# Performance work log

Hardware: AMD Instinct MI355X
Metric: run time of the kernel (lower is better)

Reference implementation:

```python
import jax, jax.numpy as jnp
import numpy as np

B, N, NPOINT, NSAMPLE = 8, 8192, 2048, 32
RADIUS = 0.4
C_IN = 64
MLP = [64, 64, 128]
EPS = 1e-5
BIG = 1e10


def setup_inputs() -> dict:
    key = jax.random.key(0)
    ks = jax.random.split(key, 2 + 4 * len(MLP))
    inp = {
        'xyz': jax.random.normal(ks[0], (B, N, 3), jnp.float32),
        'features': jax.random.normal(ks[1], (B, C_IN, N), jnp.float32),
    }
    last_c = C_IN + 3
    j = 2
    for i, out_c in enumerate(MLP):
        inp[f'w{i}'] = jax.random.normal(ks[j], (out_c, last_c), jnp.float32) * (1.0 / np.sqrt(last_c)); j += 1
        inp[f'b{i}'] = jax.random.normal(ks[j], (out_c,), jnp.float32) * 0.01; j += 1
        inp[f'g{i}'] = 1.0 + 0.01 * jax.random.normal(ks[j], (out_c,), jnp.float32); j += 1
        inp[f'bt{i}'] = 0.01 * jax.random.normal(ks[j], (out_c,), jnp.float32); j += 1
        last_c = out_c
    return inp


def fps(xyz, m):
    # Farthest point sampling; deterministic start at index 0 (torch uses randint).
    b, n, _ = xyz.shape

    def step(carry, _):
        dist, far = carry
        centroid = jnp.take_along_axis(xyz, far[:, None, None], axis=1)  # [B,1,3]
        d = jnp.sum((xyz - centroid) ** 2, axis=-1)                      # [B,N]
        dist = jnp.minimum(dist, d)
        new_far = jnp.argmax(dist, axis=1)
        return (dist, new_far), far

    init = (jnp.full((b, n), BIG, xyz.dtype), jnp.zeros((b,), jnp.int32))
    _, idxs = jax.lax.scan(step, init, None, length=m)
    return jnp.transpose(idxs)  # [B,m]


def ball_query(xyz, centroids, radius, k):
    # Euclidean cdist via the (a-b)^2 = a^2 + b^2 - 2ab expansion.
    x2 = jnp.sum(xyz * xyz, axis=-1)            # [B,N]
    c2 = jnp.sum(centroids * centroids, axis=-1)  # [B,M]
    d2 = c2[:, :, None] + x2[:, None, :] - 2.0 * jnp.einsum('bmd,bnd->bmn', centroids, xyz)
    d = jnp.sqrt(jnp.maximum(d2, 0.0))           # [B,M,N]
    dm = jnp.where(d <= radius, d, BIG)
    _, idx = jax.lax.top_k(-dm, k)               # k smallest distances
    return idx                                   # [B,M,K]


def gather_points(x, idx):
    # x: [B,N,C], idx: [B,M,K] -> [B,M,K,C]
    b = x.shape[0]
    return x[jnp.arange(b)[:, None, None], idx]


def reference(xyz, features, w0, b0, g0, bt0, w1, b1, g1, bt1, w2, b2, g2, bt2):
    idx = fps(xyz, NPOINT)                                   # [B,M]
    new_xyz = jnp.take_along_axis(xyz, idx[:, :, None], axis=1)  # [B,M,3]
    knn_idx = ball_query(xyz, new_xyz, RADIUS, NSAMPLE)      # [B,M,K]
    grouped_xyz = gather_points(xyz, knn_idx)                # [B,M,K,3]
    grouped_xyz_norm = grouped_xyz - new_xyz[:, :, None, :]
    grouped_feat = gather_points(jnp.transpose(features, (0, 2, 1)), knn_idx)  # [B,M,K,C]
    feat = jnp.concatenate([grouped_xyz_norm, grouped_feat], axis=-1)          # [B,M,K,C+3]

    for w, b, g, bt in ((w0, b0, g0, bt0), (w1, b1, g1, bt1), (w2, b2, g2, bt2)):
        feat = jnp.einsum('bmkc,oc->bmko', feat, w) + b      # 1x1 conv
        mu = jnp.mean(feat, axis=(0, 1, 2))                  # BN, training-mode batch stats
        var = jnp.mean((feat - mu) ** 2, axis=(0, 1, 2))
        feat = (feat - mu) * jax.lax.rsqrt(var + EPS) * g + bt
        feat = jax.nn.relu(feat)

    new_feat = jnp.max(feat, axis=2)                         # max over neighbors -> [B,M,C_out]
    return new_xyz, jnp.transpose(new_feat, (0, 2, 1))       # [B,M,3], [B,C_out,M]
```

## Files before the change

kernel.cpp:

```cpp
#include <hip/hip_runtime.h>
#include <hip/hip_bf16.h>
#include <stdint.h>

typedef unsigned short u16;
typedef unsigned int   u32;
typedef unsigned long long u64;
typedef float v2f __attribute__((ext_vector_type(2)));
typedef __attribute__((ext_vector_type(8))) short bf16x8;
typedef __attribute__((ext_vector_type(4))) float f32x4;

#define B_    8
#define N_    8192
#define M_    2048
#define NS_   32
#define CIN_  64
#define ROWS_ (B_*M_*NS_)
#define BIGF  1e10f
#define EPSF  1e-5f
#define INV_ROWS (1.0f/524288.0f)

__device__ __forceinline__ u16 f2bf(float f){
  u32 x=__float_as_uint(f);
  return (u16)((x + 0x7FFFu + ((x>>16)&1u))>>16);
}
__device__ __forceinline__ float bf2f(u16 u){ return __uint_as_float(((u32)u)<<16); }

__device__ __forceinline__ u64 wave_max_key(u64 k){
#define DPP_LVL(CTRL) { \
    u32 lo_=(u32)__builtin_amdgcn_update_dpp(0,(int)(u32)k,(CTRL),0xF,0xF,true); \
    u32 hi_=(u32)__builtin_amdgcn_update_dpp(0,(int)(u32)(k>>32),(CTRL),0xF,0xF,true); \
    u64 o_=((u64)hi_<<32)|(u64)lo_; \
    k=(o_>k)?o_:k; }
  DPP_LVL(0x111)
  DPP_LVL(0x112)
  DPP_LVL(0x114)
  DPP_LVL(0x118)
  DPP_LVL(0x142)
  DPP_LVL(0x143)
#undef DPP_LVL
  return k;
}

__global__ __launch_bounds__(256) void k_prep(
    const float* w0,const float* b0,const float* g0,const float* bt0,
    const float* w1,const float* b1,const float* g1,const float* bt1,
    const float* w2,const float* b2,const float* g2,const float* bt2,
    float* Wt0,float* Wt1,float* Wt2,
    float* biasf,float* gf,float* btf,float* stats,
    u16* Wb1h, u16* Wb1l)
{
  int tid=threadIdx.x;
  for (int i=tid;i<768;i+=256) stats[i]=0.f;
  for (int i=tid;i<67*64;i+=256){ int c=i>>6,o=i&63;  Wt0[c*64+o]=w0[o*67+c]; }
  for (int i=tid;i<64*64;i+=256){ int c=i>>6,o=i&63;  Wt1[c*64+o]=w1[o*64+c]; }
  for (int i=tid;i<64*128;i+=256){int c=i>>7,o=i&127; Wt2[c*128+o]=w2[o*64+c]; }
  for (int i=tid;i<4096;i+=256){
    int e=i&7, lane=(i>>3)&63, k0=(i>>9)&1, tn=i>>10;
    int col = tn*16 + (lane&15);
    int k   = k0*32 + ((lane>>4)&3)*8 + e;
    float v = w1[col*64 + k];
    u16 hib = f2bf(v);
    float lo = v - bf2f(hib);
    Wb1h[i] = hib;
    Wb1l[i] = f2bf(lo);
  }
  if (tid<64){
    biasf[0*128+tid]=b0[tid]; gf[0*128+tid]=g0[tid]; btf[0*128+tid]=bt0[tid];
    biasf[1*128+tid]=b1[tid]; gf[1*128+tid]=g1[tid]; btf[1*128+tid]=bt1[tid];
  }
  if (tid<128){
    biasf[2*128+tid]=b2[tid]; gf[2*128+tid]=g2[tid]; btf[2*128+tid]=bt2[tid];
  }
}

__global__ __launch_bounds__(256) void k_tr(const float* __restrict__ feats, u16* __restrict__ featT)
{
  __shared__ float t[64][65];
  int bb=blockIdx.y, n0=blockIdx.x*64, tid=threadIdx.x;
  int a=tid&63, q=tid>>6;
  const float* fp = feats + (size_t)bb*CIN_*N_;
  #pragma unroll
  for (int s=0;s<16;s++){ int c=q*16+s; t[c][a]=fp[(size_t)c*N_ + n0 + a]; }
  __syncthreads();
  u16* op = featT + (size_t)bb*N_*CIN_;
  #pragma unroll
  for (int s=0;s<16;s++){ int n=q*16+s; op[(size_t)(n0+n)*CIN_ + a] = f2bf(t[a][n]); }
}

__global__ __launch_bounds__(512) void k_fps(const float* __restrict__ xyz,
                                             float* __restrict__ nxyz, float* __restrict__ out0)
{
#pragma clang fp contract(off)
  __shared__ float sx[N_], sy[N_], sz[N_];
  __shared__ int sidx[M_];
  __shared__ u64 skey[2][8];
  int b=blockIdx.x, tid=threadIdx.x;
  const float* xp = xyz + (size_t)b*N_*3;
  for (int i=tid;i<N_;i+=512){ sx[i]=xp[i*3]; sy[i]=xp[i*3+1]; sz[i]=xp[i*3+2]; }
  __syncthreads();
  v2f px[8],py[8],pz[8],md[8];
  int base = tid*16;
  #pragma unroll
  for (int p=0;p<8;p++){
    px[p]=*(const v2f*)&sx[base+2*p];
    py[p]=*(const v2f*)&sy[base+2*p];
    pz[p]=*(const v2f*)&sz[base+2*p];
    v2f m0; m0[0]=BIGF; m0[1]=BIGF; md[p]=m0;
  }
  u32 invb = 0xFFFFFFFFu - (u32)base;
  int far=0;
  int lane=tid&63, wv=tid>>6;
  for (int step=0; step<M_; step++){
    if (tid==0) sidx[step]=far;
    float cxs=sx[far], cys=sy[far], czs=sz[far];
    v2f cx; cx[0]=cxs; cx[1]=cxs;
    v2f cy; cy[0]=cys; cy[1]=cys;
    v2f cz; cz[0]=czs; cz[1]=czs;
    u64 kb=0;
    #pragma unroll
    for (int p=0;p<8;p++){
      v2f dx=px[p]-cx, dy=py[p]-cy, dz=pz[p]-cz;
      v2f d=(dx*dx+dy*dy)+dz*dz;
      v2f m=__builtin_elementwise_min(md[p],d);
      md[p]=m;
      u64 k0=((u64)__float_as_uint(m[0])<<32)|(u64)(invb-(u32)(2*p));
      u64 k1=((u64)__float_as_uint(m[1])<<32)|(u64)(invb-(u32)(2*p+1));
      u64 kp=(k1>k0)?k1:k0;
      kb=(kp>kb)?kp:kb;
    }
    kb = wave_max_key(kb);
    int par = step & 1;
    if (lane==63) skey[par][wv]=kb;
    __syncthreads();
    u64 a0=skey[par][0],a1=skey[par][1],a2=skey[par][2],a3=skey[par][3];
    u64 a4=skey[par][4],a5=skey[par][5],a6=skey[par][6],a7=skey[par][7];
    a0=(a1>a0)?a1:a0; a2=(a3>a2)?a3:a2; a4=(a5>a4)?a5:a4; a6=(a7>a6)?a7:a6;
    a0=(a2>a0)?a2:a0; a4=(a6>a4)?a6:a4;
    a0=(a4>a0)?a4:a0;
    far = (int)(0xFFFFFFFFu - (u32)(a0 & 0xFFFFFFFFull));
  }
  for (int i=tid;i<M_;i+=512){
    int id = sidx[i];
    float x=sx[id], y=sy[id], z=sz[id];
    size_t o=(size_t)(b*M_+i)*3;
    nxyz[o]=x; nxyz[o+1]=y; nxyz[o+2]=z;
    out0[o]=x; out0[o+1]=y; out0[o+2]=z;
  }
}

#define BQCAP 512
__global__ __launch_bounds__(512) void k_bq(const float* __restrict__ xyz, const float* __restrict__ nxyz,
                                            int* __restrict__ knn)
{
  __shared__ float4 sP[N_];
  __shared__ float candd[8][BQCAP];
  __shared__ u16  candi[8][BQCAP];
  int tid=threadIdx.x;
  int cid0 = blockIdx.x*8;
  int b = cid0 >> 11;
  const float* xp = xyz + (size_t)b*N_*3;
  for (int i=tid;i<N_;i+=512){
    float x=xp[i*3], y=xp[i*3+1], z=xp[i*3+2];
    float x2 = __fmul_rn(x,x);
    x2 = __fadd_rn(x2, __fmul_rn(y,y));
    x2 = __fadd_rn(x2, __fmul_rn(z,z));
    sP[i]=make_float4(x,y,z,x2);
  }
  __syncthreads();
  int w=tid>>6, lane=tid&63;
  int cid = cid0 + w;
  float cx=nxyz[(size_t)cid*3], cy=nxyz[(size_t)cid*3+1], cz=nxyz[(size_t)cid*3+2];
  float c2 = __fmul_rn(cx,cx);
  c2 = __fadd_rn(c2, __fmul_rn(cy,cy));
  c2 = __fadd_rn(c2, __fmul_rn(cz,cz));
  int cnt=0;
  for (int i0=0;i0<N_;i0+=64){
    int i=i0+lane;
    float4 p=sP[i];
    float dot = __fmul_rn(cx,p.x);
    dot = __fadd_rn(dot, __fmul_rn(cy,p.y));
    dot = __fadd_rn(dot, __fmul_rn(cz,p.z));
    float d2 = __fsub_rn(__fadd_rn(c2,p.w), __fmul_rn(2.0f,dot));
    float d = sqrtf(fmaxf(d2,0.f));
    bool in = (d <= 0.4f);
    u64 msk = __ballot(in);
    int pos = cnt + __popcll(msk & ((1ull<<lane)-1ull));
    if (in && pos<BQCAP){ candd[w][pos]=d; candi[w][pos]=(u16)i; }
    cnt += __popcll(msk);
  }
  int R = cnt<BQCAP ? cnt : BQCAP;
  int* kout = knn + (size_t)cid*NS_;
  if (R >= NS_){
    for (int s=0;s<NS_;s++){
      u64 kb = ~0ull;
      for (int j=lane;j<R;j+=64){
        float v=candd[w][j];
        u64 k = ((u64)__float_as_uint(v)<<32) | (u64)(u32)j;
        kb = (k<kb)?k:kb;
      }
      u64 inv = wave_max_key(~kb);
      if (lane==63){
        u64 kw = ~inv;
        int bpp = (int)(u32)(kw & 0xFFFFFFFFull);
        kout[s]=candi[w][bpp];
        candd[w][bpp]=3e38f;
      }
    }
  } else {
    if (lane<R) kout[lane]=candi[w][lane];
    int need = NS_-R, slot = R;
    for (int i0=0; i0<N_ && need>0; i0+=64){
      int i=i0+lane;
      float4 p=sP[i];
      float dot = __fmul_rn(cx,p.x);
      dot = __fadd_rn(dot, __fmul_rn(cy,p.y));
      dot = __fadd_rn(dot, __fmul_rn(cz,p.z));
      float d2 = __fsub_rn(__fadd_rn(c2,p.w), __fmul_rn(2.0f,dot));
      float d = sqrtf(fmaxf(d2,0.f));
      bool in = (d <= 0.4f);
      u64 mm = __ballot(!in);
      while (mm && need>0){
        int bpos = __ffsll((long long)mm)-1;
        if (lane==0) kout[slot] = i0+bpos;
        slot++; need--;
        mm &= mm-1;
      }
    }
  }
}

__global__ __launch_bounds__(256) void k_mm0(const float* __restrict__ xyz, const u16* __restrict__ featT,
                                             const int* __restrict__ knn, const float* __restrict__ nxyz,
                                             const float* __restrict__ Wt0, const float* __restrict__ biasf,
                                             u16* __restrict__ Y0)
{
  __shared__ u16 Xs[256*70];
  __shared__ float Wl[67*64];
  int tid=threadIdx.x;
  for (int i=tid;i<67*64;i+=256) Wl[i]=Wt0[i];
  int base = blockIdx.x*256;
  {
    int row = base + tid;
    int bm  = row >> 5;
    int b   = row >> 16;
    int n   = knn[row];
    const float* cp = nxyz + (size_t)bm*3;
    const float* xp = xyz + ((size_t)b*N_ + n)*3;
    u16* xr = &Xs[tid*70];
    xr[0]=f2bf(xp[0]-cp[0]);
    xr[1]=f2bf(xp[1]-cp[1]);
    xr[2]=f2bf(xp[2]-cp[2]);
    const uint4* fp = (const uint4*)(featT + ((size_t)b*N_ + n)*CIN_);
    #pragma unroll
    for (int i=0;i<8;i++){
      uint4 v=fp[i];
      u16* d = xr + 3 + i*8;
      d[0]=(u16)(v.x&0xFFFFu); d[1]=(u16)(v.x>>16);
      d[2]=(u16)(v.y&0xFFFFu); d[3]=(u16)(v.y>>16);
      d[4]=(u16)(v.z&0xFFFFu); d[5]=(u16)(v.z>>16);
      d[6]=(u16)(v.w&0xFFFFu); d[7]=(u16)(v.w>>16);
    }
  }
  __syncthreads();
  int g=tid>>7, rt=tid&127;
  float acc0[32], acc1[32];
  #pragma unroll
  for (int j=0;j<32;j++){ acc0[j]=0.f; acc1[j]=0.f; }
  const u16* xa=&Xs[rt*70];
  const u16* xb=&Xs[(rt+128)*70];
  for (int c=0;c<67;c++){
    float a=bf2f(xa[c]);
    float bx=bf2f(xb[c]);
    const float4* wr=(const float4*)&Wl[c*64 + g*32];
    #pragma unroll
    for (int o=0;o<8;o++){
      float4 wv=wr[o];
      acc0[o*4+0]+=a*wv.x;  acc0[o*4+1]+=a*wv.y;  acc0[o*4+2]+=a*wv.z;  acc0[o*4+3]+=a*wv.w;
      acc1[o*4+0]+=bx*wv.x; acc1[o*4+1]+=bx*wv.y; acc1[o*4+2]+=bx*wv.z; acc1[o*4+3]+=bx*wv.w;
    }
  }
  float bb[32];
  #pragma unroll
  for (int j=0;j<32;j++) bb[j]=biasf[g*32+j];
  u16* y0p = Y0 + ((size_t)(base+rt))*64 + g*32;
  u16* y1p = Y0 + ((size_t)(base+rt+128))*64 + g*32;
  #pragma unroll
  for (int j=0;j<32;j++){
    y0p[j]=f2bf(acc0[j]+bb[j]);
    y1p[j]=f2bf(acc1[j]+bb[j]);
  }
}

template<int C>
__global__ __launch_bounds__(256) void k_stats(const u16* __restrict__ Y, float* __restrict__ statsOut)
{
  __shared__ float sred[4][128];
  int tid=threadIdx.x;
  int c0=(tid&7)*8;
  int rg=tid>>3;
  float s[8], ss[8];
  #pragma unroll
  for (int k=0;k<8;k++){ s[k]=0.f; ss[k]=0.f; }
  for (size_t r=(size_t)blockIdx.x*32+rg; r<ROWS_; r+=(size_t)gridDim.x*32){
    uint4 v=*(const uint4*)&Y[r*64+c0];
    u32 a[4]={v.x,v.y,v.z,v.w};
    #pragma unroll
    for (int q=0;q<4;q++){
      float lo=bf2f((u16)(a[q]&0xFFFFu));
      float hi=bf2f((u16)(a[q]>>16));
      s[q*2]+=lo;   ss[q*2]+=lo*lo;
      s[q*2+1]+=hi; ss[q*2+1]+=hi*hi;
    }
  }
  #pragma unroll
  for (int off=32; off>=8; off>>=1){
    #pragma unroll
    for (int k=0;k<8;k++){
      s[k]+=__shfl_down(s[k],off);
      ss[k]+=__shfl_down(ss[k],off);
    }
  }
  int lane=tid&63, wv=tid>>6;
  if (lane<8){
    #pragma unroll
    for (int k=0;k<8;k++){
      int ch=lane*8+k;
      sred[wv][ch]=s[k];
      sred[wv][64+ch]=ss[k];
    }
  }
  __syncthreads();
  if (tid<128){
    float a=sred[0][tid]+sred[1][tid]+sred[2][tid]+sred[3][tid];
    int ch=tid&63, which=tid>>6;
    atomicAdd(&statsOut[ch*2+which], a);
  }
}

__global__ __launch_bounds__(256) void k_mm1(u16* __restrict__ Y,
                                             const u16* __restrict__ Wb1h, const u16* __restrict__ Wb1l,
                                             const float* __restrict__ bias1, const float* __restrict__ gf0,
                                             const float* __restrict__ btf0, const float* __restrict__ stats0)
{
  __shared__ u16 Xs[64*64];
  __shared__ u16 WH[8*64*8];
  __shared__ u16 WL[8*64*8];
  __shared__ float sc[64], sh[64];
  int tid=threadIdx.x;
  if (tid<64){
    float mu = stats0[tid*2]*INV_ROWS;
    float var= stats0[tid*2+1]*INV_ROWS - mu*mu;
    float rs = 1.0f/sqrtf(var+EPSF);
    float s  = rs*gf0[tid];
    sc[tid]=s; sh[tid]=btf0[tid]-mu*s;
  }
  {
    const uint4* sh4=(const uint4*)Wb1h; uint4* dh4=(uint4*)WH;
    const uint4* sl4=(const uint4*)Wb1l; uint4* dl4=(uint4*)WL;
    dh4[tid]=sh4[tid]; dh4[tid+256]=sh4[tid+256];
    dl4[tid]=sl4[tid]; dl4[tid+256]=sl4[tid+256];
  }
  __syncthreads();
  size_t base=(size_t)blockIdx.x*64;
  for (int i=tid;i<512;i+=256){
    int rl=i>>3, c0=(i&7)*8;
    uint4 v=*(const uint4*)(Y + (base+rl)*64 + c0);
    u32 arr[4]={v.x,v.y,v.z,v.w};
    u32 pk[4];
    #pragma unroll
    for (int q=0;q<4;q++){
      int cc=c0+q*2;
      float lo=bf2f((u16)(arr[q]&0xFFFFu));
      float hi=bf2f((u16)(arr[q]>>16));
      lo=fmaxf(0.f, lo*sc[cc]+sh[cc]);
      hi=fmaxf(0.f, hi*sc[cc+1]+sh[cc+1]);
      pk[q] = (u32)f2bf(lo) | ((u32)f2bf(hi)<<16);
    }
    uint4 o4; o4.x=pk[0]; o4.y=pk[1]; o4.z=pk[2]; o4.w=pk[3];
    int byteoff = rl*128 + ((c0*2) ^ ((rl&7)<<4));
    *(uint4*)((char*)Xs + byteoff) = o4;
  }
  __syncthreads();
  int w=tid>>6, lane=tid&63;
  f32x4 acc[4];
  #pragma unroll
  for (int tn=0;tn<4;tn++){ acc[tn][0]=0.f; acc[tn][1]=0.f; acc[tn][2]=0.f; acc[tn][3]=0.f; }
  int arow = w*16 + (lane&15);
  #pragma unroll
  for (int k0=0;k0<2;k0++){
    int aoff = arow*128 + ((k0*64 + (lane>>4)*16) ^ ((arow&7)<<4));
    bf16x8 a = *(const bf16x8*)((const char*)Xs + aoff);
    #pragma unroll
    for (int tn=0;tn<4;tn++){
      bf16x8 bl = *(const bf16x8*)&WL[((tn*2+k0)*64+lane)*8];
      bf16x8 bh = *(const bf16x8*)&WH[((tn*2+k0)*64+lane)*8];
      acc[tn] = __builtin_amdgcn_mfma_f32_16x16x32_bf16(a, bl, acc[tn], 0,0,0);
      acc[tn] = __builtin_amdgcn_mfma_f32_16x16x32_bf16(a, bh, acc[tn], 0,0,0);
    }
  }
  #pragma unroll
  for (int tn=0;tn<4;tn++){
    int col = tn*16 + (lane&15);
    float bb = bias1[col];
    #pragma unroll
    for (int j=0;j<4;j++){
      int row = w*16 + (lane>>4)*4 + j;
      Y[(base+row)*64 + col] = f2bf(acc[tn][j] + bb);
    }
  }
}

__global__ __launch_bounds__(256) void k_mm2a(const u16* __restrict__ Y1, const float* __restrict__ Wt2,
                                              const float* __restrict__ bias2, const float* __restrict__ gf1,
                                              const float* __restrict__ btf1, const float* __restrict__ stats1,
                                              float* __restrict__ stats2, float* __restrict__ out1)
{
  __shared__ u16 Xs[128*66];
  __shared__ float Wl[64*128];
  __shared__ float sc[64], sh[64];
  __shared__ float res[4][128];
  int tid=threadIdx.x;
  if (tid<64){
    float mu = stats1[tid*2]*INV_ROWS;
    float var= stats1[tid*2+1]*INV_ROWS - mu*mu;
    float rs = 1.0f/sqrtf(var+EPSF);
    float s  = rs*gf1[tid];
    sc[tid]=s; sh[tid]=btf1[tid]-mu*s;
  }
  for (int i=tid;i<64*128;i+=256) Wl[i]=Wt2[i];
  int g=tid>>6, rt=tid&63;
  float bb[32];
  #pragma unroll
  for (int j=0;j<32;j++) bb[j]=bias2[g*32+j];
  float sSum[32], sSq[32];
  #pragma unroll
  for (int j=0;j<32;j++){ sSum[j]=0.f; sSq[j]=0.f; }
  __syncthreads();
  for (int tile=blockIdx.x; tile<4096; tile+=gridDim.x){
    size_t base=(size_t)tile*128;
    for (int i=tid;i<1024;i+=256){
      int rl=i>>3, c0=(i&7)*8;
      uint4 v=*(const uint4*)(Y1 + (base+rl)*64 + c0);
      u32 arr[4]={v.x,v.y,v.z,v.w};
      u16* d=&Xs[rl*66+c0];
      #pragma unroll
      for (int q=0;q<4;q++){
        int cc=c0+q*2;
        float lo=bf2f((u16)(arr[q]&0xFFFFu));
        float hi=bf2f((u16)(arr[q]>>16));
        lo=fmaxf(0.f, lo*sc[cc]+sh[cc]);
        hi=fmaxf(0.f, hi*sc[cc+1]+sh[cc+1]);
        d[q*2]=f2bf(lo); d[q*2+1]=f2bf(hi);
      }
    }
    __syncthreads();
    float acc0[32], acc1[32];
    #pragma unroll
    for (int j=0;j<32;j++){ acc0[j]=0.f; acc1[j]=0.f; }
    const u16* xa=&Xs[rt*66];
    const u16* xb=&Xs[(rt+64)*66];
    for (int c=0;c<64;c++){
      float a=bf2f(xa[c]);
      float bx=bf2f(xb[c]);
      const float4* wr=(const float4*)&Wl[c*128 + g*32];
      #pragma unroll
      for (int o=0;o<8;o++){
        float4 wv=wr[o];
        acc0[o*4+0]+=a*wv.x;  acc0[o*4+1]+=a*wv.y;  acc0[o*4+2]+=a*wv.z;  acc0[o*4+3]+=a*wv.w;
        acc1[o*4+0]+=bx*wv.x; acc1[o*4+1]+=bx*wv.y; acc1[o*4+2]+=bx*wv.z; acc1[o*4+3]+=bx*wv.w;
      }
    }
    #pragma unroll
    for (int j=0;j<32;j++){
      float y0=acc0[j]+bb[j], y1=acc1[j]+bb[j];
      sSum[j]+=y0+y1;
      sSq[j] +=y0*y0+y1*y1;
      float a=y0, b2=y1;
      #pragma unroll
      for (int off=16;off>0;off>>=1){
        a = fmaxf(a, __shfl_down(a, off, 32));
        b2= fmaxf(b2,__shfl_down(b2,off, 32));
      }
      if ((rt&31)==0){
        int o=g*32+j;
        res[rt>>5][o]     = a;
        res[2+(rt>>5)][o] = b2;
      }
    }
    __syncthreads();
    int bm0 = tile*4;
    for (int e=tid;e<512;e+=256){
      int gr=e>>7, o=e&127;
      int bm=bm0+gr; int bi=bm>>11, m=bm&2047;
      out1[((size_t)bi*128+o)*M_ + m] = res[gr][o];
    }
    __syncthreads();
  }
  #pragma unroll
  for (int off=32;off>0;off>>=1){
    #pragma unroll
    for (int j=0;j<32;j++){
      sSum[j]+=__shfl_down(sSum[j],off);
      sSq[j] +=__shfl_down(sSq[j],off);
    }
  }
  if (rt==0){
    #pragma unroll
    for (int j=0;j<32;j++){
      atomicAdd(&stats2[(g*32+j)*2],  sSum[j]);
      atomicAdd(&stats2[(g*32+j)*2+1],sSq[j]);
    }
  }
}

__global__ __launch_bounds__(256) void k_pool(float* __restrict__ out1, const float* __restrict__ stats2,
                                              const float* __restrict__ gf2, const float* __restrict__ btf2)
{
  int idx = blockIdx.x*256 + threadIdx.x;
  int o = (idx >> 11) & 127;
  float mu = stats2[o*2]*INV_ROWS;
  float var= stats2[o*2+1]*INV_ROWS - mu*mu;
  float rs = 1.0f/sqrtf(var+EPSF);
  float s  = rs*gf2[o];
  float sh = btf2[o]-mu*s;
  out1[idx] = fmaxf(0.f, out1[idx]*s + sh);
}

extern "C" void kernel_launch(void* const* d_in, const int* in_sizes, int n_in,
                              void* d_out, int out_size, void* d_ws, size_t ws_size,
                              hipStream_t stream)
{
  (void)in_sizes; (void)n_in; (void)out_size; (void)ws_size;
  const float* xyz =(const float*)d_in[0];
  const float* feat=(const float*)d_in[1];
  const float* w0=(const float*)d_in[2],  *b0=(const float*)d_in[3],  *g0=(const float*)d_in[4],  *bt0=(const float*)d_in[5];
  const float* w1=(const float*)d_in[6],  *b1=(const float*)d_in[7],  *g1=(const float*)d_in[8],  *bt1=(const float*)d_in[9];
  const float* w2=(const float*)d_in[10], *b2=(const float*)d_in[11], *g2=(const float*)d_in[12], *bt2=(const float*)d_in[13];
  float* out0=(float*)d_out;
  float* out1=out0 + (size_t)B_*M_*3;

  char* ws=(char*)d_ws;
  float* nxyz =(float*)(ws);
  u16*   Wb1h =(u16*)  (ws + 196608);
  u16*   Wb1l =(u16*)  (ws + 204800);
  int*   knn  =(int*)  (ws + 262144);
  float* Wt0  =(float*)(ws + 2359296);
  float* Wt1  =(float*)(ws + 2376704);
  float* Wt2  =(float*)(ws + 2393088);
  float* biasf=(float*)(ws + 2425856);
  float* gfp  =(float*)(ws + 2427392);
  float* btfp =(float*)(ws + 2428928);
  float* stats=(float*)(ws + 2430464);
  u16*   featT=(u16*)  (ws + 2433536);
  u16*   Y0   =(u16*)  (ws + 10822144);

  k_prep<<<1,256,0,stream>>>(w0,b0,g0,bt0,w1,b1,g1,bt1,w2,b2,g2,bt2,Wt0,Wt1,Wt2,biasf,gfp,btfp,stats,Wb1h,Wb1l);
  k_tr<<<dim3(128,8),256,0,stream>>>(feat, featT);
  k_fps<<<B_,512,0,stream>>>(xyz, nxyz, out0);
  k_bq<<<2048,512,0,stream>>>(xyz, nxyz, knn);
  k_mm0<<<2048,256,0,stream>>>(xyz, featT, knn, nxyz, Wt0, biasf+0, Y0);
  k_stats<64><<<128,256,0,stream>>>(Y0, stats+0);
  k_mm1<<<8192,256,0,stream>>>(Y0, Wb1h, Wb1l, biasf+128, gfp+0, btfp+0, stats+0);
  k_stats<64><<<128,256,0,stream>>>(Y0, stats+256);
  k_mm2a<<<512,256,0,stream>>>(Y0, Wt2, biasf+256, gfp+128, btfp+128, stats+256, stats+512, out1);
  k_pool<<<8192,256,0,stream>>>(out1, stats+512, gfp+256, btfp+256);
}
```

Measured before the change: 2.668 ms.

## Move final 64->128 conv to bf16 MFMA with split-weight precision and swizzled LDS

Replaces the scalar FP32 FMA loop in the last 1x1 conv kernel with bf16 MFMA 16x16x32 instructions. The weights are pre-split into high and low bf16 parts so the product keeps near-fp32 weight precision. The A tile and the output tile are stored in LDS with an XOR swizzle to avoid bank conflicts. The max-pool and BN statistics are now computed column-wise from an LDS staging buffer, with a block-level reduction before the atomics. Tiles shrink to 64 rows and LDS use grows, which may lower occupancy.

```diff
diff --git a/kernel.cpp b/kernel.cpp
--- a/kernel.cpp
+++ b/kernel.cpp
@@ -47,7 +47,7 @@
     const float* w2,const float* b2,const float* g2,const float* bt2,
     float* Wt0,float* Wt1,float* Wt2,
     float* biasf,float* gf,float* btf,float* stats,
-    u16* Wb1h, u16* Wb1l)
+    u16* Wb1h, u16* Wb1l, u16* Wb2h, u16* Wb2l)
 {
   int tid=threadIdx.x;
   for (int i=tid;i<768;i+=256) stats[i]=0.f;
@@ -60,9 +60,17 @@
     int k   = k0*32 + ((lane>>4)&3)*8 + e;
     float v = w1[col*64 + k];
     u16 hib = f2bf(v);
-    float lo = v - bf2f(hib);
     Wb1h[i] = hib;
-    Wb1l[i] = f2bf(lo);
+    Wb1l[i] = f2bf(v - bf2f(hib));
+  }
+  for (int i=tid;i<8192;i+=256){
+    int e=i&7, lane=(i>>3)&63, k0=(i>>9)&1, tn=i>>10;
+    int col = tn*16 + (lane&15);
+    int k   = k0*32 + ((lane>>4)&3)*8 + e;
+    float v = w2[col*64 + k];
+    u16 hib = f2bf(v);
+    Wb2h[i] = hib;
+    Wb2l[i] = f2bf(v - bf2f(hib));
   }
   if (tid<64){
     biasf[0*128+tid]=b0[tid]; gf[0*128+tid]=g0[tid]; btf[0*128+tid]=bt0[tid];
@@ -410,15 +418,18 @@
   }
 }
 
-__global__ __launch_bounds__(256) void k_mm2a(const u16* __restrict__ Y1, const float* __restrict__ Wt2,
+__global__ __launch_bounds__(256) void k_mm2a(const u16* __restrict__ Y1,
+                                              const u16* __restrict__ Wb2h, const u16* __restrict__ Wb2l,
                                               const float* __restrict__ bias2, const float* __restrict__ gf1,
                                               const float* __restrict__ btf1, const float* __restrict__ stats1,
                                               float* __restrict__ stats2, float* __restrict__ out1)
 {
-  __shared__ u16 Xs[128*66];
-  __shared__ float Wl[64*128];
+  __shared__ u16 Xs[64*64];
+  __shared__ u16 WH[8192];
+  __shared__ u16 WL[8192];
+  __shared__ float Ys[64*128];
   __shared__ float sc[64], sh[64];
-  __shared__ float res[4][128];
+  __shared__ float sred[512];
   int tid=threadIdx.x;
   if (tid<64){
     float mu = stats1[tid*2]*INV_ROWS;
@@ -427,22 +438,23 @@
     float s  = rs*gf1[tid];
     sc[tid]=s; sh[tid]=btf1[tid]-mu*s;
   }
-  for (int i=tid;i<64*128;i+=256) Wl[i]=Wt2[i];
-  int g=tid>>6, rt=tid&63;
-  float bb[32];
-  #pragma unroll
-  for (int j=0;j<32;j++) bb[j]=bias2[g*32+j];
-  float sSum[32], sSq[32];
-  #pragma unroll
-  for (int j=0;j<32;j++){ sSum[j]=0.f; sSq[j]=0.f; }
-  __syncthreads();
-  for (int tile=blockIdx.x; tile<4096; tile+=gridDim.x){
-    size_t base=(size_t)tile*128;
-    for (int i=tid;i<1024;i+=256){
+  {
+    const uint4* s4=(const uint4*)Wb2h; uint4* d4=(uint4*)WH;
+    const uint4* s5=(const uint4*)Wb2l; uint4* d5=(uint4*)WL;
+    for (int i=tid;i<1024;i+=256){ d4[i]=s4[i]; d5[i]=s5[i]; }
+  }
+  int w=tid>>6, lane=tid&63;
+  int pg=tid>>7, po=tid&127;
+  float bias_po_unused; (void)bias_po_unused;
+  float accSum=0.f, accSq=0.f;
+  __syncthreads();
+  for (int tile=blockIdx.x; tile<8192; tile+=gridDim.x){
+    size_t base=(size_t)tile*64;
+    for (int i=tid;i<512;i+=256){
       int rl=i>>3, c0=(i&7)*8;
       uint4 v=*(const uint4*)(Y1 + (base+rl)*64 + c0);
       u32 arr[4]={v.x,v.y,v.z,v.w};
-      u16* d=&Xs[rl*66+c0];
+      u32 pk[4];
       #pragma unroll
       for (int q=0;q<4;q++){
         int cc=c0+q*2;
@@ -450,66 +462,64 @@
         float hi=bf2f((u16)(arr[q]>>16));
         lo=fmaxf(0.f, lo*sc[cc]+sh[cc]);
         hi=fmaxf(0.f, hi*sc[cc+1]+sh[cc+1]);
-        d[q*2]=f2bf(lo); d[q*2+1]=f2bf(hi);
-      }
+        pk[q] = (u32)f2bf(lo) | ((u32)f2bf(hi)<<16);
+      }
+      uint4 o4; o4.x=pk[0]; o4.y=pk[1]; o4.z=pk[2]; o4.w=pk[3];
+      int byteoff = rl*128 + ((c0*2) ^ ((rl&7)<<4));
+      *(uint4*)((char*)Xs + byteoff) = o4;
     }
     __syncthreads();
-    float acc0[32], acc1[32];
-    #pragma unroll
-    for (int j=0;j<32;j++){ acc0[j]=0.f; acc1[j]=0.f; }
-    const u16* xa=&Xs[rt*66];
-    const u16* xb=&Xs[(rt+64)*66];
-    for (int c=0;c<64;c++){
-      float a=bf2f(xa[c]);
-      float bx=bf2f(xb[c]);
-      const float4* wr=(const float4*)&Wl[c*128 + g*32];
+    f32x4 acc[8];
+    #pragma unroll
+    for (int tn=0;tn<8;tn++){ acc[tn][0]=0.f; acc[tn][1]=0.f; acc[tn][2]=0.f; acc[tn][3]=0.f; }
+    int arow = w*16 + (lane&15);
+    #pragma unroll
+    for (int k0=0;k0<2;k0++){
+      int aoff = arow*128 + ((k0*64 + (lane>>4)*16) ^ ((arow&7)<<4));
+      bf16x8 a = *(const bf16x8*)((const char*)Xs + aoff);
       #pragma unroll
-      for (int o=0;o<8;o++){
-        float4 wv=wr[o];
-        acc0[o*4+0]+=a*wv.x;  acc0[o*4+1]+=a*wv.y;  acc0[o*4+2]+=a*wv.z;  acc0[o*4+3]+=a*wv.w;
-        acc1[o*4+0]+=bx*wv.x; acc1[o*4+1]+=bx*wv.y; acc1[o*4+2]+=bx*wv.z; acc1[o*4+3]+=bx*wv.w;
-      }
-    }
-    #pragma unroll
-    for (int j=0;j<32;j++){
-      float y0=acc0[j]+bb[j], y1=acc1[j]+bb[j];
-      sSum[j]+=y0+y1;
-      sSq[j] +=y0*y0+y1*y1;
-      float a=y0, b2=y1;
+      for (int tn=0;tn<8;tn++){
+        bf16x8 bl = *(const bf16x8*)&WL[((tn*2+k0)*64+lane)*8];
+        bf16x8 bh = *(const bf16x8*)&WH[((tn*2+k0)*64+lane)*8];
+        acc[tn] = __builtin_amdgcn_mfma_f32_16x16x32_bf16(a, bl, acc[tn], 0,0,0);
+        acc[tn] = __builtin_amdgcn_mfma_f32_16x16x32_bf16(a, bh, acc[tn], 0,0,0);
+      }
+    }
+    #pragma unroll
+    for (int tn=0;tn<8;tn++){
+      int col = tn*16 + (lane&15);
+      float bb = bias2[col];
       #pragma unroll
-      for (int off=16;off>0;off>>=1){
-        a = fmaxf(a, __shfl_down(a, off, 32));
-        b2= fmaxf(b2,__shfl_down(b2,off, 32));
-      }
-      if ((rt&31)==0){
-        int o=g*32+j;
-        res[rt>>5][o]     = a;
-        res[2+(rt>>5)][o] = b2;
+      for (int j=0;j<4;j++){
+        int row = w*16 + (lane>>4)*4 + j;
+        int byteoff = row*512 + ((col*4) ^ ((row&7)<<4));
+        *(float*)((char*)Ys + byteoff) = acc[tn][j] + bb;
       }
     }
     __syncthreads();
-    int bm0 = tile*4;
-    for (int e=tid;e<512;e+=256){
-      int gr=e>>7, o=e&127;
-      int bm=bm0+gr; int bi=bm>>11, m=bm&2047;
-      out1[((size_t)bi*128+o)*M_ + m] = res[gr][o];
+    {
+      float mx=-3e38f;
+      #pragma unroll 4
+      for (int k=0;k<32;k++){
+        int row = pg*32 + k;
+        int byteoff = row*512 + ((po*4) ^ ((row&7)<<4));
+        float y = *(const float*)((const char*)Ys + byteoff);
+        accSum += y; accSq += y*y;
+        mx = fmaxf(mx, y);
+      }
+      int bm = tile*2 + pg; int bi = bm>>11, m = bm&2047;
+      out1[((size_t)bi*128+po)*M_ + m] = mx;
     }
     __syncthreads();
   }
-  #pragma unroll
-  for (int off=32;off>0;off>>=1){
-    #pragma unroll
-    for (int j=0;j<32;j++){
-      sSum[j]+=__shfl_down(sSum[j],off);
-      sSq[j] +=__shfl_down(sSq[j],off);
-    }
-  }
-  if (rt==0){
-    #pragma unroll
-    for (int j=0;j<32;j++){
-      atomicAdd(&stats2[(g*32+j)*2],  sSum[j]);
-      atomicAdd(&stats2[(g*32+j)*2+1],sSq[j]);
-    }
+  sred[tid]      = accSum;
+  sred[256+tid]  = accSq;
+  __syncthreads();
+  if (tid<128){
+    float s = sred[tid] + sred[tid+128];
+    float q = sred[256+tid] + sred[256+tid+128];
+    atomicAdd(&stats2[tid*2],   s);
+    atomicAdd(&stats2[tid*2+1], q);
   }
 }
 
@@ -543,6 +553,8 @@
   float* nxyz =(float*)(ws);
   u16*   Wb1h =(u16*)  (ws + 196608);
   u16*   Wb1l =(u16*)  (ws + 204800);
+  u16*   Wb2h =(u16*)  (ws + 212992);
+  u16*   Wb2l =(u16*)  (ws + 229376);
   int*   knn  =(int*)  (ws + 262144);
   float* Wt0  =(float*)(ws + 2359296);
   float* Wt1  =(float*)(ws + 2376704);
@@ -554,7 +566,8 @@
   u16*   featT=(u16*)  (ws + 2433536);
   u16*   Y0   =(u16*)  (ws + 10822144);
 
-  k_prep<<<1,256,0,stream>>>(w0,b0,g0,bt0,w1,b1,g1,bt1,w2,b2,g2,bt2,Wt0,Wt1,Wt2,biasf,gfp,btfp,stats,Wb1h,Wb1l);
+  k_prep<<<1,256,0,stream>>>(w0,b0,g0,bt0,w1,b1,g1,bt1,w2,b2,g2,bt2,Wt0,Wt1,Wt2,biasf,gfp,btfp,stats,
+                             Wb1h,Wb1l,Wb2h,Wb2l);
   k_tr<<<dim3(128,8),256,0,stream>>>(feat, featT);
   k_fps<<<B_,512,0,stream>>>(xyz, nxyz, out0);
   k_bq<<<2048,512,0,stream>>>(xyz, nxyz, knn);
@@ -562,6 +575,6 @@
   k_stats<64><<<128,256,0,stream>>>(Y0, stats+0);
   k_mm1<<<8192,256,0,stream>>>(Y0, Wb1h, Wb1l, biasf+128, gfp+0, btfp+0, stats+0);
   k_stats<64><<<128,256,0,stream>>>(Y0, stats+256);
-  k_mm2a<<<512,256,0,stream>>>(Y0, Wt2, biasf+256, gfp+128, btfp+128, stats+256, stats+512, out1);
+  k_mm2a<<<512,256,0,stream>>>(Y0, Wb2h, Wb2l, biasf+256, gfp+128, btfp+128, stats+256, stats+512, out1);
   k_pool<<<8192,256,0,stream>>>(out1, stats+512, gfp+256, btfp+256);
 }
```

Measured after the change: 2.360 ms. -11.5%, faster.
